# Performance work log

Measured on AMD Instinct MI355X. Metric: run time of the kernel, lower is better.

The kernel has to match this reference:

```python
import jax, jax.numpy as jnp
import numpy as np
from math import pi

K_MAX = 0.1   # init k
DLT_K = 0.02  # init dk
EPS = 0.1

N_IMG, N_ATOM = 32, 400000


def _dot(a, b):
    # sum over last two dims, keepdims -> shape [..., 1, 1]
    return jnp.sum(a * b, axis=(-2, -1), keepdims=True)


def _norm(a):
    return jnp.sqrt(_dot(a, a))


def setup_inputs() -> dict:
    key = jax.random.key(0)
    k1, k2, k3 = jax.random.split(key, 3)
    pos = jax.random.normal(k1, (N_IMG, N_ATOM, 3), dtype=jnp.float32)
    frc = jax.random.normal(k2, (N_IMG, N_ATOM, 3), dtype=jnp.float32)
    eng = jax.random.normal(k3, (N_IMG,), dtype=jnp.float32)
    # ensure climbing-image argmax lies in the interior (valid frc_para index)
    eng = eng.at[N_IMG // 2].add(10.0)
    return {"pos": pos, "frc": frc, "eng": eng}


def reference(pos, frc, eng):
    dtype = pos.dtype
    eng3 = eng[:, None, None]  # [N,1,1]

    # ---- spring force k per segment: [N-1,1,1] ----
    eng_ref = jnp.min(eng3) - EPS
    eng_max = jnp.max(eng3)
    eng_i = jnp.maximum(eng3[1:], eng3[:-1])
    k = K_MAX - DLT_K * (eng_max - eng_i) / (eng_max - eng_ref)
    k = jnp.where(eng_i < eng_ref, K_MAX - DLT_K, k)

    # ---- improved tangent estimation: [N-2, A, 3] ----
    tau_p = pos[1:-1] - pos[:-2]
    tau_m = pos[2:] - pos[1:-1]
    e0, e1, e2 = eng3[:-2], eng3[1:-1], eng3[2:]
    msk_pp = ((e2 > e1) & (e1 > e0)).astype(dtype)
    msk_mm = ((e2 < e1) & (e1 < e0)).astype(dtype)
    not_both = 1.0 - jnp.maximum(msk_pp, msk_mm)
    msk_p = (e2 > e1).astype(dtype) * not_both
    msk_m = (e2 < e1).astype(dtype) * not_both
    dv_max = jnp.maximum(jnp.abs(e2 - e1), jnp.abs(e0 - e1))
    dv_min = jnp.minimum(jnp.abs(e2 - e1), jnp.abs(e0 - e1))
    tau = (tau_p * msk_pp + tau_m * msk_mm
           + (tau_p * dv_max + tau_m * dv_min) * msk_p
           + (tau_p * dv_min + tau_m * dv_max) * msk_m)
    tau = tau / _norm(tau)

    # ---- NEB force decomposition ----
    frc_in = frc[1:-1]
    vecp = pos[2:] - pos[1:-1]
    vecm = pos[1:-1] - pos[:-2]
    frc_para = _dot(frc_in, tau) * tau
    spr = k[1:] * vecp - k[:-1] * vecm
    spr_para = (k[1:] * _norm(vecp) - k[:-1] * _norm(vecm)) * tau
    frc_perp = frc_in - frc_para  # uses pre-climbing frc_para (torch in-place order)
    spr_perp = spr - spr_para

    # climbing image: double parallel force at the highest-energy image
    i = jnp.argmax(eng) - 1  # eng index -> frc_para index offset (interior images)
    # torch indexes frc_para with the raw eng argmax; reproduce that indexing
    i_raw = jnp.argmax(eng)
    frc_para = frc_para.at[i_raw].multiply(2.0)

    frc_neb = spr_para - frc_para  # nudged=True

    # doubly nudged switch term
    sw = (2.0 / pi) * jnp.arctan2(_dot(frc_perp, frc_perp), _dot(spr_perp, spr_perp))
    doubly = spr_perp - _dot(spr_perp, frc_perp) * frc_perp * sw
    frc_neb = frc_neb + doubly

    out_frc = frc + jnp.pad(frc_neb, ((1, 1), (0, 0), (0, 0)))
    return out_frc
```

## Files before the change

### kernel.cpp

```cpp
#include <hip/hip_runtime.h>
#include <math.h>

#define N_IMG 32
#define N_ATOM 400000
#define NE (N_ATOM*3)
#define NE4 (NE/4)
#define KMAXC 0.1f
#define DLTKC 0.02f
#define EPSE 0.1f

#define OFF_SDD 0
#define OFF_SPM 31
#define OFF_SFP 61
#define OFF_SFM 91
#define OFF_SFF 121
#define NSUM 151
#define OFF_CO  160
#define OFF_PART 256
#define NBXPP 592

#define NBXP 586
#define NBX2 1172
#define NCHUNK 5

__device__ __forceinline__ float dot4(float4 a, float4 b) {
    return a.x*b.x + a.y*b.y + a.z*b.z + a.w*b.w;
}
__device__ __forceinline__ float4 sub4(float4 a, float4 b) {
    return make_float4(a.x-b.x, a.y-b.y, a.z-b.z, a.w-b.w);
}

__device__ __forceinline__ float wred_dpp(float x) {
    x += __int_as_float(__builtin_amdgcn_update_dpp(0, __float_as_int(x), 0x111, 0xf, 0xf, false));
    x += __int_as_float(__builtin_amdgcn_update_dpp(0, __float_as_int(x), 0x112, 0xf, 0xf, false));
    x += __int_as_float(__builtin_amdgcn_update_dpp(0, __float_as_int(x), 0x114, 0xf, 0xf, false));
    x += __int_as_float(__builtin_amdgcn_update_dpp(0, __float_as_int(x), 0x118, 0xf, 0xf, false));
    x += __int_as_float(__builtin_amdgcn_update_dpp(0, __float_as_int(x), 0x142, 0xa, 0xf, false));
    x += __int_as_float(__builtin_amdgcn_update_dpp(0, __float_as_int(x), 0x143, 0xc, 0xf, false));
    return x;
}

__global__ __launch_bounds__(256)
__attribute__((amdgpu_waves_per_eu(4, 4)))
void eb_pass1(const float* __restrict__ pos,
              const float* __restrict__ frc,
              float* __restrict__ part) {
    const int c = blockIdx.y;
    const int j0 = 1 + 6 * c;
    const float4* pos4 = reinterpret_cast<const float4*>(pos);
    const float4* frc4 = reinterpret_cast<const float4*>(frc);

    float sdd[7], spm[6], sfp[6], sfm[6], sff[6];
#pragma unroll
    for (int i = 0; i < 7; ++i) sdd[i] = 0.f;
#pragma unroll
    for (int i = 0; i < 6; ++i) { spm[i] = 0.f; sfp[i] = 0.f; sfm[i] = 0.f; sff[i] = 0.f; }

    for (int t = blockIdx.x * 256 + threadIdx.x; t < NE4; t += 256 * NBXP) {
        float4 p[8], f[6];
#pragma unroll
        for (int i = 0; i < 8; ++i) p[i] = pos4[(size_t)(j0 - 1 + i) * NE4 + t];
#pragma unroll
        for (int i = 0; i < 6; ++i) f[i] = frc4[(size_t)(j0 + i) * NE4 + t];
        float4 d[7];
#pragma unroll
        for (int i = 0; i < 7; ++i) d[i] = sub4(p[i + 1], p[i]);
#pragma unroll
        for (int i = 0; i < 7; ++i) sdd[i] += dot4(d[i], d[i]);
#pragma unroll
        for (int jj = 0; jj < 6; ++jj) {
            spm[jj] += dot4(d[jj], d[jj + 1]);
            sfp[jj] += dot4(f[jj], d[jj]);
            sfm[jj] += dot4(f[jj], d[jj + 1]);
            sff[jj] += dot4(f[jj], f[jj]);
        }
    }

    float v[31];
#pragma unroll
    for (int i = 0; i < 7; ++i) v[i] = sdd[i];
#pragma unroll
    for (int i = 0; i < 6; ++i) { v[7 + i] = spm[i]; v[13 + i] = sfp[i]; v[19 + i] = sfm[i]; v[25 + i] = sff[i]; }

    __shared__ float red[4][31];
    const int wave = threadIdx.x >> 6;
    const int lane = threadIdx.x & 63;
#pragma unroll
    for (int s = 0; s < 31; ++s) {
        float r = wred_dpp(v[s]);
        if (lane == 63) red[wave][s] = r;
    }
    __syncthreads();
    const int s = threadIdx.x;
    if (s < 31) {
        float r = red[0][s] + red[1][s] + red[2][s] + red[3][s];
        int slot; bool owned = true;
        if (s < 7)       { owned = (s < 6) || (c == NCHUNK - 1); slot = OFF_SDD + (j0 - 1) + s; }
        else if (s < 13) slot = OFF_SPM + (j0 - 1) + (s - 7);
        else if (s < 19) slot = OFF_SFP + (j0 - 1) + (s - 13);
        else if (s < 25) slot = OFF_SFM + (j0 - 1) + (s - 19);
        else             slot = OFF_SFF + (j0 - 1) + (s - 25);
        if (owned) part[(size_t)slot * NBXPP + blockIdx.x] = r;
    }
}

__global__ __launch_bounds__(256) void eb_reduce(const float* __restrict__ part,
                                                 float* __restrict__ sums) {
    const int s = blockIdx.x;
    float acc = 0.f;
    for (int r = threadIdx.x; r < NBXP; r += 256)
        acc += part[(size_t)s * NBXPP + r];
    __shared__ float red[4];
    const int wave = threadIdx.x >> 6;
    const int lane = threadIdx.x & 63;
    float v = wred_dpp(acc);
    if (lane == 63) red[wave] = v;
    __syncthreads();
    if (threadIdx.x == 0) sums[s] = red[0] + red[1] + red[2] + red[3];
}

__global__ void eb_coeff(const float* __restrict__ eng,
                         const float* __restrict__ sums,
                         float* __restrict__ co) {
    const int jj = threadIdx.x;
    if (jj >= N_IMG - 2 || blockIdx.x != 0) return;
    float e[N_IMG];
    float emin = 1e30f, emax = -1e30f;
    int imax = 0;
    for (int i = 0; i < N_IMG; ++i) {
        float v = eng[i];
        e[i] = v;
        if (v < emin) emin = v;
        if (v > emax) { emax = v; imax = i; }
    }
    const float eref = emin - EPSE;
    float e0 = e[jj], e1 = e[jj + 1], e2 = e[jj + 2];
    float eim = fmaxf(e1, e0);
    float km = KMAXC - DLTKC * (emax - eim) / (emax - eref);
    if (eim < eref) km = KMAXC - DLTKC;
    float eip = fmaxf(e2, e1);
    float kp = KMAXC - DLTKC * (emax - eip) / (emax - eref);
    if (eip < eref) kp = KMAXC - DLTKC;

    float pp = (e2 > e1 && e1 > e0) ? 1.f : 0.f;
    float mm = (e2 < e1 && e1 < e0) ? 1.f : 0.f;
    float nb = 1.f - fmaxf(pp, mm);
    float mp = ((e2 > e1) ? 1.f : 0.f) * nb;
    float mq = ((e2 < e1) ? 1.f : 0.f) * nb;
    float dvmax = fmaxf(fabsf(e2 - e1), fabsf(e0 - e1));
    float dvmin = fminf(fabsf(e2 - e1), fabsf(e0 - e1));
    float a = pp + dvmax * mp + dvmin * mq;
    float b = mm + dvmin * mp + dvmax * mq;
    float Spp = sums[OFF_SDD + jj];
    float Smm = sums[OFF_SDD + jj + 1];
    float Spm = sums[OFF_SPM + jj];
    float Sfp = sums[OFF_SFP + jj];
    float Sfm = sums[OFF_SFM + jj];
    float Sff = sums[OFF_SFF + jj];
    float ntau2 = a * a * Spp + 2.f * a * b * Spm + b * b * Smm;
    float ntau = sqrtf(ntau2);
    float ta = a / ntau, tb = b / ntau;
    float fpar = ta * Sfp + tb * Sfm;
    float spar = kp * sqrtf(Smm) - km * sqrtf(Spp);
    float ffpp = Sff - fpar * fpar;
    float strau = ta * (kp * Spm - km * Spp) + tb * (kp * Smm - km * Spm);
    float Sss = kp * kp * Smm - 2.f * kp * km * Spm + km * km * Spp;
    float sspp = Sss - 2.f * spar * strau + spar * spar;
    float Ssf = kp * Sfm - km * Sfp;
    float spfp = Ssf - fpar * strau;
    float sw = (2.0f / 3.14159265358979323846f) * atan2f(ffpp, sspp);
    float cc = spfp * sw;
    float g = (jj == imax) ? 2.f : 1.f;
    float w = (cc - g) * fpar / ntau;
    co[jj]      = 1.f - cc;
    co[30 + jj] = kp + w * b;
    co[60 + jj] = w * a - km;
}

__global__ __launch_bounds__(256)
__attribute__((amdgpu_waves_per_eu(4, 4)))
void eb_pass2(const float* __restrict__ pos,
              const float* __restrict__ frc,
              const float* __restrict__ co,
              float* __restrict__ out) {
    __shared__ float A[30], B[30], C[30];
    if (threadIdx.x < 30) {
        A[threadIdx.x] = co[threadIdx.x];
        B[threadIdx.x] = co[30 + threadIdx.x];
        C[threadIdx.x] = co[60 + threadIdx.x];
    }
    __syncthreads();
    const int t = blockIdx.x * 256 + threadIdx.x;
    if (t >= NE4) return;
    const int c = blockIdx.y;
    const int j0 = 1 + 6 * c;
    const float4* pos4 = reinterpret_cast<const float4*>(pos);
    const float4* frc4 = reinterpret_cast<const float4*>(frc);
    float4* out4 = reinterpret_cast<float4*>(out);

    float4 p[8], f[6];
#pragma unroll
    for (int i = 0; i < 8; ++i) p[i] = pos4[(size_t)(j0 - 1 + i) * NE4 + t];
#pragma unroll
    for (int i = 0; i < 6; ++i) f[i] = frc4[(size_t)(j0 + i) * NE4 + t];

    if (c == 0) out4[t] = frc4[t];
    if (c == NCHUNK - 1) {
        size_t i31 = (size_t)31 * NE4 + t;
        out4[i31] = frc4[i31];
    }

    float4 d[7];
#pragma unroll
    for (int i = 0; i < 7; ++i) d[i] = sub4(p[i + 1], p[i]);
#pragma unroll
    for (int jj = 0; jj < 6; ++jj) {
        const int j = j0 + jj;
        const int g = j - 1;
        float ca = A[g], cb = B[g], cd = C[g];
        float4 o;
        o.x = ca * f[jj].x + cb * d[jj + 1].x + cd * d[jj].x;
        o.y = ca * f[jj].y + cb * d[jj + 1].y + cd * d[jj].y;
        o.z = ca * f[jj].z + cb * d[jj + 1].z + cd * d[jj].z;
        o.w = ca * f[jj].w + cb * d[jj + 1].w + cd * d[jj].w;
        out4[(size_t)j * NE4 + t] = o;
    }
}

extern "C" void kernel_launch(void* const* d_in, const int* in_sizes, int n_in,
                              void* d_out, int out_size, void* d_ws, size_t ws_size,
                              hipStream_t stream) {
    const float* pos = (const float*)d_in[0];
    const float* frc = (const float*)d_in[1];
    const float* eng = (const float*)d_in[2];
    float* out = (float*)d_out;
    float* ws = (float*)d_ws;
    float* sums = ws;
    float* co   = ws + OFF_CO;
    float* part = ws + OFF_PART;

    eb_pass1<<<dim3(NBXP, NCHUNK), 256, 0, stream>>>(pos, frc, part);
    eb_reduce<<<NSUM, 256, 0, stream>>>(part, sums);
    eb_coeff<<<1, 64, 0, stream>>>(eng, sums, co);
    eb_pass2<<<dim3(NBX2, NCHUNK), 256, 0, stream>>>(pos, frc, co, out);
}
```

Before: 420.5 us.

## Fuse reduce and coefficient kernels into pass1 via last-block atomic counter

Pass1 now increments a global atomic counter after writing its per-block partial sums. The last block to finish reduces all partials and computes the per-image coefficients, which removes two separate kernel launches and their dependency gaps. A memset is added to reset the counter on each call, and the amdgpu_waves_per_eu attributes are dropped from both streaming kernels. The risks are a serial tail where one block does the full reduction, the cost of the memset, and possible register or occupancy changes from removing the waves_per_eu hint.

```diff
diff --git a/kernel.cpp b/kernel.cpp
--- a/kernel.cpp
+++ b/kernel.cpp
@@ -9,19 +9,21 @@
 #define DLTKC 0.02f
 #define EPSE 0.1f
 
+#define OFF_CO  160
+#define OFF_CTR 250
+#define OFF_PART 256
+#define NSUM 151
 #define OFF_SDD 0
 #define OFF_SPM 31
 #define OFF_SFP 61
 #define OFF_SFM 91
 #define OFF_SFF 121
-#define NSUM 151
-#define OFF_CO  160
-#define OFF_PART 256
 #define NBXPP 592
 
 #define NBXP 586
 #define NBX2 1172
 #define NCHUNK 5
+#define TOTB (NBXP * NCHUNK)
 
 __device__ __forceinline__ float dot4(float4 a, float4 b) {
     return a.x*b.x + a.y*b.y + a.z*b.z + a.w*b.w;
@@ -40,11 +42,12 @@
     return x;
 }
 
-__global__ __launch_bounds__(256)
-__attribute__((amdgpu_waves_per_eu(4, 4)))
-void eb_pass1(const float* __restrict__ pos,
-              const float* __restrict__ frc,
-              float* __restrict__ part) {
+__global__ __launch_bounds__(256) void eb_pass1r(const float* __restrict__ pos,
+                                                 const float* __restrict__ frc,
+                                                 const float* __restrict__ eng,
+                                                 float* __restrict__ part,
+                                                 float* __restrict__ co,
+                                                 unsigned int* __restrict__ counter) {
     const int c = blockIdx.y;
     const int j0 = 1 + 6 * c;
     const float4* pos4 = reinterpret_cast<const float4*>(pos);
@@ -83,106 +86,115 @@
     for (int i = 0; i < 6; ++i) { v[7 + i] = spm[i]; v[13 + i] = sfp[i]; v[19 + i] = sfm[i]; v[25 + i] = sff[i]; }
 
     __shared__ float red[4][31];
-    const int wave = threadIdx.x >> 6;
-    const int lane = threadIdx.x & 63;
-#pragma unroll
-    for (int s = 0; s < 31; ++s) {
-        float r = wred_dpp(v[s]);
-        if (lane == 63) red[wave][s] = r;
-    }
-    __syncthreads();
-    const int s = threadIdx.x;
-    if (s < 31) {
-        float r = red[0][s] + red[1][s] + red[2][s] + red[3][s];
-        int slot; bool owned = true;
-        if (s < 7)       { owned = (s < 6) || (c == NCHUNK - 1); slot = OFF_SDD + (j0 - 1) + s; }
-        else if (s < 13) slot = OFF_SPM + (j0 - 1) + (s - 7);
-        else if (s < 19) slot = OFF_SFP + (j0 - 1) + (s - 13);
-        else if (s < 25) slot = OFF_SFM + (j0 - 1) + (s - 19);
-        else             slot = OFF_SFF + (j0 - 1) + (s - 25);
-        if (owned) part[(size_t)slot * NBXPP + blockIdx.x] = r;
-    }
-}
-
-__global__ __launch_bounds__(256) void eb_reduce(const float* __restrict__ part,
-                                                 float* __restrict__ sums) {
-    const int s = blockIdx.x;
-    float acc = 0.f;
-    for (int r = threadIdx.x; r < NBXP; r += 256)
-        acc += part[(size_t)s * NBXPP + r];
-    __shared__ float red[4];
-    const int wave = threadIdx.x >> 6;
-    const int lane = threadIdx.x & 63;
-    float v = wred_dpp(acc);
-    if (lane == 63) red[wave] = v;
-    __syncthreads();
-    if (threadIdx.x == 0) sums[s] = red[0] + red[1] + red[2] + red[3];
-}
-
-__global__ void eb_coeff(const float* __restrict__ eng,
-                         const float* __restrict__ sums,
-                         float* __restrict__ co) {
-    const int jj = threadIdx.x;
-    if (jj >= N_IMG - 2 || blockIdx.x != 0) return;
-    float e[N_IMG];
-    float emin = 1e30f, emax = -1e30f;
-    int imax = 0;
-    for (int i = 0; i < N_IMG; ++i) {
-        float v = eng[i];
-        e[i] = v;
-        if (v < emin) emin = v;
-        if (v > emax) { emax = v; imax = i; }
-    }
-    const float eref = emin - EPSE;
-    float e0 = e[jj], e1 = e[jj + 1], e2 = e[jj + 2];
-    float eim = fmaxf(e1, e0);
-    float km = KMAXC - DLTKC * (emax - eim) / (emax - eref);
-    if (eim < eref) km = KMAXC - DLTKC;
-    float eip = fmaxf(e2, e1);
-    float kp = KMAXC - DLTKC * (emax - eip) / (emax - eref);
-    if (eip < eref) kp = KMAXC - DLTKC;
-
-    float pp = (e2 > e1 && e1 > e0) ? 1.f : 0.f;
-    float mm = (e2 < e1 && e1 < e0) ? 1.f : 0.f;
-    float nb = 1.f - fmaxf(pp, mm);
-    float mp = ((e2 > e1) ? 1.f : 0.f) * nb;
-    float mq = ((e2 < e1) ? 1.f : 0.f) * nb;
-    float dvmax = fmaxf(fabsf(e2 - e1), fabsf(e0 - e1));
-    float dvmin = fminf(fabsf(e2 - e1), fabsf(e0 - e1));
-    float a = pp + dvmax * mp + dvmin * mq;
-    float b = mm + dvmin * mp + dvmax * mq;
-    float Spp = sums[OFF_SDD + jj];
-    float Smm = sums[OFF_SDD + jj + 1];
-    float Spm = sums[OFF_SPM + jj];
-    float Sfp = sums[OFF_SFP + jj];
-    float Sfm = sums[OFF_SFM + jj];
-    float Sff = sums[OFF_SFF + jj];
-    float ntau2 = a * a * Spp + 2.f * a * b * Spm + b * b * Smm;
-    float ntau = sqrtf(ntau2);
-    float ta = a / ntau, tb = b / ntau;
-    float fpar = ta * Sfp + tb * Sfm;
-    float spar = kp * sqrtf(Smm) - km * sqrtf(Spp);
-    float ffpp = Sff - fpar * fpar;
-    float strau = ta * (kp * Spm - km * Spp) + tb * (kp * Smm - km * Spm);
-    float Sss = kp * kp * Smm - 2.f * kp * km * Spm + km * km * Spp;
-    float sspp = Sss - 2.f * spar * strau + spar * spar;
-    float Ssf = kp * Sfm - km * Sfp;
-    float spfp = Ssf - fpar * strau;
-    float sw = (2.0f / 3.14159265358979323846f) * atan2f(ffpp, sspp);
-    float cc = spfp * sw;
-    float g = (jj == imax) ? 2.f : 1.f;
-    float w = (cc - g) * fpar / ntau;
-    co[jj]      = 1.f - cc;
-    co[30 + jj] = kp + w * b;
-    co[60 + jj] = w * a - km;
-}
-
-__global__ __launch_bounds__(256)
-__attribute__((amdgpu_waves_per_eu(4, 4)))
-void eb_pass2(const float* __restrict__ pos,
-              const float* __restrict__ frc,
-              const float* __restrict__ co,
-              float* __restrict__ out) {
+    {
+        const int wave = threadIdx.x >> 6;
+        const int lane = threadIdx.x & 63;
+#pragma unroll
+        for (int s = 0; s < 31; ++s) {
+            float r = wred_dpp(v[s]);
+            if (lane == 63) red[wave][s] = r;
+        }
+    }
+    __syncthreads();
+    {
+        const int s = threadIdx.x;
+        if (s < 31) {
+            float r = red[0][s] + red[1][s] + red[2][s] + red[3][s];
+            int slot; bool owned = true;
+            if (s < 7)       { owned = (s < 6) || (c == NCHUNK - 1); slot = OFF_SDD + (j0 - 1) + s; }
+            else if (s < 13) slot = OFF_SPM + (j0 - 1) + (s - 7);
+            else if (s < 19) slot = OFF_SFP + (j0 - 1) + (s - 13);
+            else if (s < 25) slot = OFF_SFM + (j0 - 1) + (s - 19);
+            else             slot = OFF_SFF + (j0 - 1) + (s - 25);
+            if (owned) part[(size_t)slot * NBXPP + blockIdx.x] = r;
+        }
+    }
+
+    __threadfence();
+    __syncthreads();
+    __shared__ int lastFlag;
+    if (threadIdx.x == 0) {
+        unsigned int old = atomicAdd(counter, 1u);
+        lastFlag = (old == (unsigned)(TOTB - 1)) ? 1 : 0;
+    }
+    __syncthreads();
+    if (!lastFlag) return;
+    __threadfence();
+
+    __shared__ float ssum[NSUM];
+    {
+        const int wave = threadIdx.x >> 6;
+        const int lane = threadIdx.x & 63;
+        for (int s = wave; s < NSUM; s += 4) {
+            float acc = 0.f;
+            for (int r = lane; r < NBXP; r += 64)
+                acc += part[(size_t)s * NBXPP + r];
+            float t = wred_dpp(acc);
+            if (lane == 63) ssum[s] = t;
+        }
+    }
+    __syncthreads();
+
+    if (threadIdx.x < N_IMG - 2) {
+        const int jj = threadIdx.x;
+        float e[N_IMG];
+        float emin = 1e30f, emax = -1e30f;
+        int imax = 0;
+        for (int i = 0; i < N_IMG; ++i) {
+            float vv = eng[i];
+            e[i] = vv;
+            if (vv < emin) emin = vv;
+            if (vv > emax) { emax = vv; imax = i; }
+        }
+        const float eref = emin - EPSE;
+        float e0 = e[jj], e1 = e[jj + 1], e2 = e[jj + 2];
+        float eim = fmaxf(e1, e0);
+        float km = KMAXC - DLTKC * (emax - eim) / (emax - eref);
+        if (eim < eref) km = KMAXC - DLTKC;
+        float eip = fmaxf(e2, e1);
+        float kp = KMAXC - DLTKC * (emax - eip) / (emax - eref);
+        if (eip < eref) kp = KMAXC - DLTKC;
+
+        float pp = (e2 > e1 && e1 > e0) ? 1.f : 0.f;
+        float mm = (e2 < e1 && e1 < e0) ? 1.f : 0.f;
+        float nb = 1.f - fmaxf(pp, mm);
+        float mp = ((e2 > e1) ? 1.f : 0.f) * nb;
+        float mq = ((e2 < e1) ? 1.f : 0.f) * nb;
+        float dvmax = fmaxf(fabsf(e2 - e1), fabsf(e0 - e1));
+        float dvmin = fminf(fabsf(e2 - e1), fabsf(e0 - e1));
+        float a = pp + dvmax * mp + dvmin * mq;
+        float bb = mm + dvmin * mp + dvmax * mq;
+        float Spp = ssum[OFF_SDD + jj];
+        float Smm = ssum[OFF_SDD + jj + 1];
+        float Spm = ssum[OFF_SPM + jj];
+        float Sfp = ssum[OFF_SFP + jj];
+        float Sfm = ssum[OFF_SFM + jj];
+        float Sff = ssum[OFF_SFF + jj];
+        float ntau2 = a * a * Spp + 2.f * a * bb * Spm + bb * bb * Smm;
+        float ntau = sqrtf(ntau2);
+        float ta = a / ntau, tb = bb / ntau;
+        float fpar = ta * Sfp + tb * Sfm;
+        float spar = kp * sqrtf(Smm) - km * sqrtf(Spp);
+        float ffpp = Sff - fpar * fpar;
+        float strau = ta * (kp * Spm - km * Spp) + tb * (kp * Smm - km * Spm);
+        float Sss = kp * kp * Smm - 2.f * kp * km * Spm + km * km * Spp;
+        float sspp = Sss - 2.f * spar * strau + spar * spar;
+        float Ssf = kp * Sfm - km * Sfp;
+        float spfp = Ssf - fpar * strau;
+        float sw = (2.0f / 3.14159265358979323846f) * atan2f(ffpp, sspp);
+        float cc = spfp * sw;
+        float g = (jj == imax) ? 2.f : 1.f;
+        float w = (cc - g) * fpar / ntau;
+        co[jj]      = 1.f - cc;
+        co[30 + jj] = kp + w * bb;
+        co[60 + jj] = w * a - km;
+    }
+}
+
+__global__ __launch_bounds__(256) void eb_pass2(const float* __restrict__ pos,
+                                                const float* __restrict__ frc,
+                                                const float* __restrict__ co,
+                                                float* __restrict__ out) {
     __shared__ float A[30], B[30], C[30];
     if (threadIdx.x < 30) {
         A[threadIdx.x] = co[threadIdx.x];
@@ -235,12 +247,12 @@
     const float* eng = (const float*)d_in[2];
     float* out = (float*)d_out;
     float* ws = (float*)d_ws;
-    float* sums = ws;
     float* co   = ws + OFF_CO;
+    unsigned int* counter = (unsigned int*)(ws + OFF_CTR);
     float* part = ws + OFF_PART;
 
-    eb_pass1<<<dim3(NBXP, NCHUNK), 256, 0, stream>>>(pos, frc, part);
-    eb_reduce<<<NSUM, 256, 0, stream>>>(part, sums);
-    eb_coeff<<<1, 64, 0, stream>>>(eng, sums, co);
+    hipMemsetAsync(counter, 0, sizeof(unsigned int), stream);
+
+    eb_pass1r<<<dim3(NBXP, NCHUNK), 256, 0, stream>>>(pos, frc, eng, part, co, counter);
     eb_pass2<<<dim3(NBX2, NCHUNK), 256, 0, stream>>>(pos, frc, co, out);
 }
```

Measured after the change: 893.6 us. 2.12x slower.
